# Optimization experiments

Measured on AMD Instinct MI355X. Metric: run time of the kernel, lower is better.

Reference implementation:

```python
import jax, jax.numpy as jnp
import numpy as np

B, N, D_POINTS, D_MODEL = 2, 2048, 32, 512


def _gather(feat, idx):
    # feat: [B, N, C], idx: [B, N, K] -> [B, N, K, C]
    return jax.vmap(lambda f, i: f[i])(feat, idx)


def setup_inputs() -> dict:
    key = jax.random.key(0)
    ks = jax.random.split(key, 20)
    def lin(k, fan_in, fan_out):
        bound = 1.0 / np.sqrt(fan_in)
        return jax.random.uniform(k, (fan_in, fan_out), jnp.float32, -bound, bound)
    def bias(k, fan_in, fan_out):
        bound = 1.0 / np.sqrt(fan_in)
        return jax.random.uniform(k, (fan_out,), jnp.float32, -bound, bound)
    return {
        "xyz": jax.random.normal(ks[0], (B, N, 3), jnp.float32),
        "points": jax.random.normal(ks[1], (B, N, D_POINTS), jnp.float32),
        "fc1_w": lin(ks[2], D_POINTS, D_MODEL), "fc1_b": bias(ks[3], D_POINTS, D_MODEL),
        "fc2_w": lin(ks[4], D_MODEL, D_POINTS), "fc2_b": bias(ks[5], D_MODEL, D_POINTS),
        "delta_w1": lin(ks[6], 3, D_MODEL), "delta_b1": bias(ks[7], 3, D_MODEL),
        "delta_w2": lin(ks[8], D_MODEL, D_MODEL), "delta_b2": bias(ks[9], D_MODEL, D_MODEL),
        "gamma_w1": lin(ks[10], D_MODEL, D_MODEL), "gamma_b1": bias(ks[11], D_MODEL, D_MODEL),
        "gamma_w2": lin(ks[12], D_MODEL, D_MODEL), "gamma_b2": bias(ks[13], D_MODEL, D_MODEL),
        "wq": lin(ks[14], D_MODEL, D_MODEL),
        "wk": lin(ks[15], D_MODEL, D_MODEL),
        "wv": lin(ks[16], D_MODEL, D_MODEL),
        "knn_k": 16,
    }


def reference(xyz, points, fc1_w, fc1_b, fc2_w, fc2_b,
              delta_w1, delta_b1, delta_w2, delta_b2,
              gamma_w1, gamma_b1, gamma_w2, gamma_b2,
              wq, wk, wv, knn_k):
    # square_distance: [B, N, N]
    sq = jnp.sum(xyz * xyz, axis=-1)
    dists = sq[:, :, None] + sq[:, None, :] - 2.0 * jnp.einsum('bnc,bmc->bnm', xyz, xyz)
    # knn: k smallest distances (argsort[:, :, :k] equivalent)
    _, knn_idx = jax.lax.top_k(-dists, knn_k)           # [B, N, K]
    knn_xyz = _gather(xyz, knn_idx)                      # [B, N, K, 3]

    pre = points
    x = points @ fc1_w + fc1_b                           # [B, N, d_model]
    q = x @ wq                                           # [B, N, d_model]
    k = _gather(x @ wk, knn_idx)                         # [B, N, K, d_model]
    v = _gather(x @ wv, knn_idx)                         # [B, N, K, d_model]

    # positional encoding MLP on delta xyz
    delta = xyz[:, :, None, :] - knn_xyz                 # [B, N, K, 3]
    pos_enc = jax.nn.relu(delta @ delta_w1 + delta_b1) @ delta_w2 + delta_b2

    # gamma MLP on (q - k + pos_enc)
    a = q[:, :, None, :] - k + pos_enc
    a = jax.nn.relu(a @ gamma_w1 + gamma_b1) @ gamma_w2 + gamma_b2

    scale = jnp.asarray(np.sqrt(D_MODEL), a.dtype)
    attn = jax.nn.softmax(a / scale, axis=-2)            # softmax over neighbors, per channel

    res = jnp.sum(attn * (v + pos_enc), axis=2)          # einsum 'bmnf,bmnf->bmf'
    res = res @ fc2_w + fc2_b + pre                      # [B, N, d_points]
    return res, attn
```

## Files before the change

kernel.cpp:

```cpp
#include <hip/hip_runtime.h>
#include <hip/hip_bf16.h>
#include <math.h>

typedef __bf16 bf16_t;
typedef float f32x4 __attribute__((ext_vector_type(4)));
typedef bf16_t bf16x8 __attribute__((ext_vector_type(8)));

#define BM 128
#define BN 128
#define BKT 32
#define NT 16

#define GLD_LDS16(gp, lp) __builtin_amdgcn_global_load_lds( \
    (const __attribute__((address_space(1))) void*)(gp), \
    (__attribute__((address_space(3))) void*)(lp), 16, 0, 0)

struct TC7 { const float* src[7]; bf16_t* dst[7]; };
__global__ __launch_bounds__(256) void tcast7_kernel(TC7 tc) {
  int job = blockIdx.x >> 10;
  int idx = (blockIdx.x & 1023) * 256 + threadIdx.x;
  if (job < 6) {
    int n = idx >> 9, k = idx & 511;
    tc.dst[job][idx] = (bf16_t)tc.src[job][k * 512 + n];
  } else {
    tc.dst[job][idx] = (bf16_t)tc.src[job][idx];
  }
}

__global__ __launch_bounds__(256) void cc_kernel(const float* __restrict__ db2, const float* __restrict__ gw1,
                                                 const float* __restrict__ gb1, float* __restrict__ cc) {
  int n = blockIdx.x * 256 + threadIdx.x;
  float s = gb1[n];
  for (int d = 0; d < 512; ++d) s = fmaf(db2[d], gw1[d * 512 + n], s);
  cc[n] = s;
}

__global__ __launch_bounds__(256) void knn_kernel(const float* __restrict__ xyz, int* __restrict__ knn) {
  __shared__ float sx[2048], sy[2048], sz[2048], sq[2048];
  int tid = threadIdx.x;
  int lane = tid & 63, wave = tid >> 6;
  int gq = blockIdx.x * 4 + wave;
  int b  = gq >> 11;
  int base = b << 11;
  for (int p = tid; p < 2048; p += 256) {
    float x = xyz[(base + p) * 3 + 0];
    float y = xyz[(base + p) * 3 + 1];
    float z = xyz[(base + p) * 3 + 2];
    sx[p] = x; sy[p] = y; sz[p] = z;
    sq[p] = __fadd_rn(__fadd_rn(__fmul_rn(x, x), __fmul_rn(y, y)), __fmul_rn(z, z));
  }
  __syncthreads();
  int iq = gq & 2047;
  float qx = sx[iq], qy = sy[iq], qz = sz[iq], sqi = sq[iq];

  unsigned long long key[32];
  #pragma unroll
  for (int j = 0; j < 32; ++j) {
    int p = lane + j * 64;
    float d = __fmul_rn(sx[p], qx);
    d = fmaf(sy[p], qy, d);
    d = fmaf(sz[p], qz, d);
    float dist = __fsub_rn(__fadd_rn(sqi, sq[p]), __fmul_rn(2.0f, d));
    unsigned int bits = __float_as_uint(dist);
    unsigned int sk = bits ^ (unsigned int)(((int)bits >> 31) | 0x80000000);
    key[j] = ((unsigned long long)sk << 32) | (unsigned int)p;
  }

  int r = 0;
  #pragma unroll 1
  for (int s = 0; s < 16; ++s) {
    unsigned long long m = key[0];
    #pragma unroll
    for (int j = 1; j < 32; ++j) m = (key[j] < m) ? key[j] : m;
    #pragma unroll
    for (int off = 32; off > 0; off >>= 1) {
      unsigned long long o = (unsigned long long)__shfl_xor((long long)m, off);
      if (o < m) m = o;
    }
    if (lane == s) r = base + (int)(m & 0xFFFFFFFFu);
    #pragma unroll
    for (int j = 0; j < 32; ++j) key[j] = (key[j] == m) ? ~0ULL : key[j];
  }
  if (lane < 16) knn[gq * 16 + lane] = r;
}

__global__ __launch_bounds__(256) void xfeat_kernel(const float* __restrict__ points, const float* __restrict__ fc1_w,
                                                    const float* __restrict__ fc1_b, bf16_t* __restrict__ xb) {
  __shared__ float p[32];
  int m = blockIdx.x, tid = threadIdx.x;
  if (tid < 32) p[tid] = points[m * 32 + tid];
  __syncthreads();
  for (int c = tid; c < 512; c += 256) {
    float a = fc1_b[c];
    #pragma unroll
    for (int kk = 0; kk < 32; ++kk) a = fmaf(p[kk], fc1_w[kk * 512 + c], a);
    xb[m * 512 + c] = (bf16_t)a;
  }
}

__global__ __launch_bounds__(256) void final_kernel(const float* __restrict__ res_mid, const float* __restrict__ fc2_w,
                                                    const float* __restrict__ fc2_b, const float* __restrict__ points,
                                                    float* __restrict__ out) {
  int oid = blockIdx.x * 256 + threadIdx.x;
  int m = oid >> 5, c = oid & 31;
  float a = fc2_b[c];
  const float* rm = res_mid + m * 512;
  for (int kk = 0; kk < 512; ++kk) a = fmaf(rm[kk], fc2_w[kk * 32 + c], a);
  out[oid] = a + points[oid];
}

struct GP {
  const bf16_t* A; const bf16_t* Bt; const bf16_t* Bt2;
  bf16_t* Cb; float* Cf; const float* bias; int ldc;
  const float* xyz; const int* knn; const float* dw1; const float* db1;
  const float* cc; const bf16_t* qkg;
  const bf16_t* vb; float* pe_attn; float* res_mid;
};

template <int SRC, int EPI>
__global__ __launch_bounds__(256) void gemm_kernel(GP gp) {
  __shared__ bf16_t Alds[2 * BM * BKT];
  __shared__ bf16_t Blds[2 * BN * BKT];
  __shared__ bf16_t B2lds[(EPI == 5) ? (2 * BN * BKT) : 8];
  __shared__ float  wl[(SRC == 2) ? 4 * 512 : 8];
  int tid  = threadIdx.x;
  int lane = tid & 63, wave = tid >> 6;
  int wr = wave >> 1, wc = wave & 1;
  int lr = lane & 15, lg = lane >> 4;

  int gx = gridDim.x;
  int nwg = gx * gridDim.y;
  int orig = blockIdx.y * gx + blockIdx.x;
  int cpx = nwg >> 3;
  int swz = (orig & 7) * cpx + (orig >> 3);
  int bx = swz % gx;
  int by = swz / gx;
  int n0 = bx * BN, m0 = by * BM;

  f32x4 acc[4][4];
  f32x4 acc2[(EPI == 5) ? 4 : 1][4];
  #pragma unroll
  for (int i = 0; i < 4; ++i)
    #pragma unroll
    for (int j = 0; j < 4; ++j) {
      acc[i][j] = (f32x4){0.f, 0.f, 0.f, 0.f};
      if (EPI == 5) acc2[i][j] = (f32x4){0.f, 0.f, 0.f, 0.f};
    }

  int rS2 = tid >> 2;
  int sl  = tid & 3;
  int swb = (rS2 >> 1) & 3;
  int scS = ((sl ^ swb) << 3);

  float dx0, dy0, dz0, dx1, dy1, dz1;
  if (SRC == 2) {
    for (int c = tid; c < 512; c += 256) {
      wl[c]        = gp.dw1[c];
      wl[512 + c]  = gp.dw1[512 + c];
      wl[1024 + c] = gp.dw1[1024 + c];
      wl[1536 + c] = gp.db1[c];
    }
    int m_a = m0 + rS2, m_b = m0 + rS2 + 64;
    int ga = m_a >> 4, ja = gp.knn[m_a];
    int gb = m_b >> 4, jb = gp.knn[m_b];
    dx0 = gp.xyz[ga * 3 + 0] - gp.xyz[ja * 3 + 0];
    dy0 = gp.xyz[ga * 3 + 1] - gp.xyz[ja * 3 + 1];
    dz0 = gp.xyz[ga * 3 + 2] - gp.xyz[ja * 3 + 2];
    dx1 = gp.xyz[gb * 3 + 0] - gp.xyz[jb * 3 + 0];
    dy1 = gp.xyz[gb * 3 + 1] - gp.xyz[jb * 3 + 1];
    dz1 = gp.xyz[gb * 3 + 2] - gp.xyz[jb * 3 + 2];
    __syncthreads();
  }

  auto stageA = [&](int t, int buf) {
    int k0 = t * BKT;
    if (SRC == 0) {
      GLD_LDS16(gp.A + (size_t)(m0 + rS2) * 512 + k0 + scS,       Alds + buf * (BM * BKT) + tid * 8);
      GLD_LDS16(gp.A + (size_t)(m0 + 64 + rS2) * 512 + k0 + scS,  Alds + buf * (BM * BKT) + 2048 + tid * 8);
    } else {
      int cb = k0 + sl * 8;
      f32x4 w0a = *(const f32x4*)(&wl[cb]),        w0b = *(const f32x4*)(&wl[cb + 4]);
      f32x4 w1a = *(const f32x4*)(&wl[512 + cb]),  w1b = *(const f32x4*)(&wl[512 + cb + 4]);
      f32x4 w2a = *(const f32x4*)(&wl[1024 + cb]), w2b = *(const f32x4*)(&wl[1024 + cb + 4]);
      f32x4 bba = *(const f32x4*)(&wl[1536 + cb]), bbb = *(const f32x4*)(&wl[1536 + cb + 4]);
      bf16_t* Ab = Alds + buf * (BM * BKT);
      bf16x8 o;
      #pragma unroll
      for (int u = 0; u < 4; ++u) {
        float h = fmaf(dz0, w2a[u], fmaf(dy0, w1a[u], dx0 * w0a[u])) + bba[u];
        o[u] = (bf16_t)fmaxf(h, 0.0f);
      }
      #pragma unroll
      for (int u = 0; u < 4; ++u) {
        float h = fmaf(dz0, w2b[u], fmaf(dy0, w1b[u], dx0 * w0b[u])) + bbb[u];
        o[4 + u] = (bf16_t)fmaxf(h, 0.0f);
      }
      *(bf16x8*)(&Ab[rS2 * BKT + ((sl ^ swb) << 3)]) = o;
      #pragma unroll
      for (int u = 0; u < 4; ++u) {
        float h = fmaf(dz1, w2a[u], fmaf(dy1, w1a[u], dx1 * w0a[u])) + bba[u];
        o[u] = (bf16_t)fmaxf(h, 0.0f);
      }
      #pragma unroll
      for (int u = 0; u < 4; ++u) {
        float h = fmaf(dz1, w2b[u], fmaf(dy1, w1b[u], dx1 * w0b[u])) + bbb[u];
        o[4 + u] = (bf16_t)fmaxf(h, 0.0f);
      }
      *(bf16x8*)(&Ab[(rS2 + 64) * BKT + ((sl ^ swb) << 3)]) = o;
    }
  };
  auto stageB = [&](int t, int buf) {
    int k0 = t * BKT;
    GLD_LDS16(gp.Bt + (size_t)(n0 + rS2) * 512 + k0 + scS,       Blds + buf * (BN * BKT) + tid * 8);
    GLD_LDS16(gp.Bt + (size_t)(n0 + 64 + rS2) * 512 + k0 + scS,  Blds + buf * (BN * BKT) + 2048 + tid * 8);
    if (EPI == 5) {
      GLD_LDS16(gp.Bt2 + (size_t)(n0 + rS2) * 512 + k0 + scS,      B2lds + buf * (BN * BKT) + tid * 8);
      GLD_LDS16(gp.Bt2 + (size_t)(n0 + 64 + rS2) * 512 + k0 + scS, B2lds + buf * (BN * BKT) + 2048 + tid * 8);
    }
  };

  stageA(0, 0);
  stageB(0, 0);

  #pragma unroll 1
  for (int t = 0; t < NT; ++t) {
    int cur = t & 1;
    if (t + 1 < NT) {
      stageA(t + 1, cur ^ 1);
      stageB(t + 1, cur ^ 1);
      if (SRC == 0) {
        if (EPI == 5) asm volatile("s_waitcnt vmcnt(6)" ::: "memory");
        else          asm volatile("s_waitcnt vmcnt(4)" ::: "memory");
      } else {
        if (EPI == 5) asm volatile("s_waitcnt vmcnt(4) lgkmcnt(0)" ::: "memory");
        else          asm volatile("s_waitcnt vmcnt(2) lgkmcnt(0)" ::: "memory");
      }
    } else {
      asm volatile("s_waitcnt vmcnt(0) lgkmcnt(0)" ::: "memory");
    }
    __builtin_amdgcn_s_barrier();

    const bf16_t* Ab = Alds + cur * (BM * BKT);
    const bf16_t* Bb = Blds + cur * (BN * BKT);
    const bf16_t* B2b = B2lds + cur * (BN * BKT);
    bf16x8 af[4], bfr[4], b2r[4];
    #pragma unroll
    for (int mi = 0; mi < 4; ++mi) {
      int rr = wr * 64 + mi * 16 + lr;
      af[mi] = *(const bf16x8*)(&Ab[rr * BKT + ((lg ^ ((rr >> 1) & 3)) << 3)]);
    }
    #pragma unroll
    for (int nj = 0; nj < 4; ++nj) {
      int rr = wc * 64 + nj * 16 + lr;
      bfr[nj] = *(const bf16x8*)(&Bb[rr * BKT + ((lg ^ ((rr >> 1) & 3)) << 3)]);
      if (EPI == 5) b2r[nj] = *(const bf16x8*)(&B2b[rr * BKT + ((lg ^ ((rr >> 1) & 3)) << 3)]);
    }
    #pragma unroll
    for (int mi = 0; mi < 4; ++mi)
      #pragma unroll
      for (int nj = 0; nj < 4; ++nj) {
        acc[mi][nj] = __builtin_amdgcn_mfma_f32_16x16x32_bf16(af[mi], bfr[nj], acc[mi][nj], 0, 0, 0);
        if (EPI == 5)
          acc2[mi][nj] = __builtin_amdgcn_mfma_f32_16x16x32_bf16(af[mi], b2r[nj], acc2[mi][nj], 0, 0, 0);
      }
    __builtin_amdgcn_s_barrier();
  }

  if (EPI == 4) {
    #pragma unroll
    for (int mi = 0; mi < 4; ++mi)
      #pragma unroll
      for (int nj = 0; nj < 4; ++nj) {
        int col = n0 + wc * 64 + nj * 16 + lr;
        #pragma unroll
        for (int r = 0; r < 4; ++r) {
          int row = m0 + wr * 64 + mi * 16 + lg * 4 + r;
          gp.Cb[(size_t)col * 512 + row] = (bf16_t)acc[mi][nj][r];
        }
      }
  } else if (EPI == 6) {
    #pragma unroll
    for (int mi = 0; mi < 4; ++mi)
      #pragma unroll
      for (int nj = 0; nj < 4; ++nj) {
        int col = n0 + wc * 64 + nj * 16 + lr;
        int part = col >> 9, c = col & 511;
        #pragma unroll
        for (int r = 0; r < 4; ++r) {
          int row = m0 + wr * 64 + mi * 16 + lg * 4 + r;
          gp.Cb[((size_t)part * 4096 + row) * 512 + c] = (bf16_t)acc[mi][nj][r];
        }
      }
  } else if (EPI == 7) {
    #pragma unroll
    for (int mi = 0; mi < 4; ++mi)
      #pragma unroll
      for (int nj = 0; nj < 4; ++nj) {
        int col = n0 + wc * 64 + nj * 16 + lr;
        #pragma unroll
        for (int r = 0; r < 4; ++r) {
          int row = m0 + wr * 64 + mi * 16 + lg * 4 + r;
          gp.Cb[(size_t)row * gp.ldc + col] = (bf16_t)acc[mi][nj][r];
        }
      }
  } else if (EPI == 5) {
    #pragma unroll
    for (int mi = 0; mi < 4; ++mi) {
      int g = (m0 + wr * 64 + mi * 16) >> 4;
      #pragma unroll
      for (int nj = 0; nj < 4; ++nj) {
        int col = n0 + wc * 64 + nj * 16 + lr;
        float db2v = gp.bias[col];
        float ccv  = gp.cc[col];
        float qgv  = (float)gp.qkg[(size_t)g * 512 + col];
        #pragma unroll
        for (int r = 0; r < 4; ++r) {
          int row = m0 + wr * 64 + mi * 16 + lg * 4 + r;
          gp.Cf[(size_t)row * 512 + col] = acc[mi][nj][r] + db2v;
          int j = gp.knn[row];
          float kgv = (float)gp.qkg[(size_t)(4096 + j) * 512 + col];
          float hv = acc2[mi][nj][r] + ccv + qgv - kgv;
          gp.Cb[(size_t)row * 512 + col] = (bf16_t)fmaxf(hv, 0.0f);
        }
      }
    }
  } else {
    const float scale = 22.62741699796952f;
    #pragma unroll
    for (int mi = 0; mi < 4; ++mi) {
      int g = (m0 + wr * 64 + mi * 16) >> 4;
      #pragma unroll
      for (int nj = 0; nj < 4; ++nj) {
        int col = n0 + wc * 64 + nj * 16 + lr;
        float sv[4];
        float mx = -INFINITY;
        #pragma unroll
        for (int r = 0; r < 4; ++r) {
          sv[r] = (acc[mi][nj][r] + gp.bias[col]) / scale;
          mx = fmaxf(mx, sv[r]);
        }
        mx = fmaxf(mx, __shfl_xor(mx, 16));
        mx = fmaxf(mx, __shfl_xor(mx, 32));
        float e[4], sum = 0.f;
        #pragma unroll
        for (int r = 0; r < 4; ++r) { e[r] = expf(sv[r] - mx); sum += e[r]; }
        sum += __shfl_xor(sum, 16);
        sum += __shfl_xor(sum, 32);
        float part = 0.f;
        #pragma unroll
        for (int r = 0; r < 4; ++r) {
          int row = g * 16 + lg * 4 + r;
          float at = e[r] / sum;
          int j = gp.knn[row];
          float vv  = (float)gp.vb[(size_t)j * 512 + col];
          float pev = gp.pe_attn[(size_t)row * 512 + col];
          part = fmaf(at, vv + pev, part);
          gp.pe_attn[(size_t)row * 512 + col] = at;
        }
        part += __shfl_xor(part, 16);
        part += __shfl_xor(part, 32);
        if (lg == 0) gp.res_mid[(size_t)g * 512 + col] = part;
      }
    }
  }
}

extern "C" void kernel_launch(void* const* d_in, const int* in_sizes, int n_in,
                              void* d_out, int out_size, void* d_ws, size_t ws_size,
                              hipStream_t stream) {
  const float* xyz    = (const float*)d_in[0];
  const float* points = (const float*)d_in[1];
  const float* fc1_w  = (const float*)d_in[2];
  const float* fc1_b  = (const float*)d_in[3];
  const float* fc2_w  = (const float*)d_in[4];
  const float* fc2_b  = (const float*)d_in[5];
  const float* dw1    = (const float*)d_in[6];
  const float* db1    = (const float*)d_in[7];
  const float* dw2    = (const float*)d_in[8];
  const float* db2    = (const float*)d_in[9];
  const float* gw1    = (const float*)d_in[10];
  const float* gb1    = (const float*)d_in[11];
  const float* gw2    = (const float*)d_in[12];
  const float* gb2    = (const float*)d_in[13];
  const float* wq     = (const float*)d_in[14];
  const float* wk     = (const float*)d_in[15];
  const float* wv     = (const float*)d_in[16];

  float* out = (float*)d_out;
  float* attn_pe = out + 131072;

  char* w = (char*)d_ws;
  bf16_t* wqkvT  = (bf16_t*)w; w += (size_t)1536 * 512 * 2;
  bf16_t* dw2T   = (bf16_t*)w; w += (size_t)512 * 512 * 2;
  bf16_t* gw1T   = (bf16_t*)w; w += (size_t)512 * 512 * 2;
  bf16_t* gw2T   = (bf16_t*)w; w += (size_t)512 * 512 * 2;
  bf16_t* dw2b   = (bf16_t*)w; w += (size_t)512 * 512 * 2;
  bf16_t* WpT    = (bf16_t*)w; w += (size_t)512 * 512 * 2;
  float*  cc     = (float*)w;  w += (size_t)512 * 4;
  int*    knn    = (int*)w;    w += (size_t)65536 * 4;
  bf16_t* xb     = (bf16_t*)w; w += (size_t)4096 * 512 * 2;
  bf16_t* qkvb   = (bf16_t*)w; w += (size_t)3 * 4096 * 512 * 2;
  bf16_t* qkg    = (bf16_t*)w; w += (size_t)2 * 4096 * 512 * 2;
  bf16_t* h2     = (bf16_t*)w; w += (size_t)65536 * 512 * 2;
  float*  res_mid= (float*)w;  w += (size_t)4096 * 512 * 4;

  TC7 tc;
  tc.src[0] = wq;  tc.dst[0] = wqkvT;
  tc.src[1] = wk;  tc.dst[1] = wqkvT + 512 * 512;
  tc.src[2] = wv;  tc.dst[2] = wqkvT + 2 * 512 * 512;
  tc.src[3] = dw2; tc.dst[3] = dw2T;
  tc.src[4] = gw1; tc.dst[4] = gw1T;
  tc.src[5] = gw2; tc.dst[5] = gw2T;
  tc.src[6] = dw2; tc.dst[6] = dw2b;
  tcast7_kernel<<<7168, 256, 0, stream>>>(tc);

  knn_kernel<<<1024, 256, 0, stream>>>(xyz, knn);
  xfeat_kernel<<<4096, 256, 0, stream>>>(points, fc1_w, fc1_b, xb);
  cc_kernel<<<2, 256, 0, stream>>>(db2, gw1, gb1, cc);

  GP gp{};
  gp.A = dw2b; gp.Bt = gw1T; gp.Cb = WpT; gp.ldc = 512;
  gemm_kernel<0, 4><<<dim3(4, 4), 256, 0, stream>>>(gp);

  GP gq{};
  gq.A = xb; gq.Bt = wqkvT; gq.Cb = qkvb; gq.ldc = 1536;
  gemm_kernel<0, 6><<<dim3(12, 32), 256, 0, stream>>>(gq);

  GP gk{};
  gk.A = qkvb; gk.Bt = gw1T; gk.Cb = qkg; gk.ldc = 512;
  gemm_kernel<0, 7><<<dim3(4, 64), 256, 0, stream>>>(gk);

  GP gd{};
  gd.Bt = dw2T; gd.Bt2 = WpT; gd.Cf = attn_pe; gd.Cb = h2; gd.bias = db2;
  gd.xyz = xyz; gd.knn = knn; gd.dw1 = dw1; gd.db1 = db1;
  gd.cc = cc; gd.qkg = qkg;
  gemm_kernel<2, 5><<<dim3(4, 512), 256, 0, stream>>>(gd);

  GP gs{};
  gs.A = h2; gs.Bt = gw2T; gs.bias = gb2;
  gs.knn = knn; gs.vb = qkvb + (size_t)2 * 4096 * 512; gs.pe_attn = attn_pe; gs.res_mid = res_mid;
  gemm_kernel<0, 3><<<dim3(4, 512), 256, 0, stream>>>(gs);

  final_kernel<<<512, 256, 0, stream>>>(res_mid, fc2_w, fc2_b, points, out);
}
```

Baseline: 504.9 us.

## Fold gamma_w1 into Wq/Wk weights and drop the separate qk-gamma GEMM

Precomputes Wq·Gw1 and Wk·Gw1 as weight products in the small batched weight GEMM (alongside dw2·Gw1), so the QKV GEMM directly emits v, q·Gw1 and k·Gw1. This removes the intermediate GEMM over the 4096-row q/k activations and its launch. The main loop is restructured: the SRC==2 path issues its computed A staging after the MFMA phase, with raised wave priority during the MFMAs, to overlap VALU with matrix work. Rounding the fused weight products to bf16 slightly changes numerics.

```diff
diff --git a/kernel.cpp b/kernel.cpp
--- a/kernel.cpp
+++ b/kernel.cpp
@@ -19,7 +19,7 @@
 __global__ __launch_bounds__(256) void tcast7_kernel(TC7 tc) {
   int job = blockIdx.x >> 10;
   int idx = (blockIdx.x & 1023) * 256 + threadIdx.x;
-  if (job < 6) {
+  if (job < 4) {
     int n = idx >> 9, k = idx & 511;
     tc.dst[job][idx] = (bf16_t)tc.src[job][k * 512 + n];
   } else {
@@ -115,6 +115,7 @@
   const float* xyz; const int* knn; const float* dw1; const float* db1;
   const float* cc; const bf16_t* qkg;
   const bf16_t* vb; float* pe_attn; float* res_mid;
+  const bf16_t* Aj[3]; bf16_t* Cbj[3];
 };
 
 template <int SRC, int EPI>
@@ -135,7 +136,9 @@
   int swz = (orig & 7) * cpx + (orig >> 3);
   int bx = swz % gx;
   int by = swz / gx;
-  int n0 = bx * BN, m0 = by * BM;
+  int n0 = bx * BN;
+  int m0 = ((EPI == 4) ? (by & 3) : by) * BM;
+  const bf16_t* Aptr = (EPI == 4) ? gp.Aj[by >> 2] : gp.A;
 
   f32x4 acc[4][4];
   f32x4 acc2[(EPI == 5) ? 4 : 1][4];
@@ -175,8 +178,8 @@
   auto stageA = [&](int t, int buf) {
     int k0 = t * BKT;
     if (SRC == 0) {
-      GLD_LDS16(gp.A + (size_t)(m0 + rS2) * 512 + k0 + scS,       Alds + buf * (BM * BKT) + tid * 8);
-      GLD_LDS16(gp.A + (size_t)(m0 + 64 + rS2) * 512 + k0 + scS,  Alds + buf * (BM * BKT) + 2048 + tid * 8);
+      GLD_LDS16(Aptr + (size_t)(m0 + rS2) * 512 + k0 + scS,       Alds + buf * (BM * BKT) + tid * 8);
+      GLD_LDS16(Aptr + (size_t)(m0 + 64 + rS2) * 512 + k0 + scS,  Alds + buf * (BM * BKT) + 2048 + tid * 8);
     } else {
       int cb = k0 + sl * 8;
       f32x4 w0a = *(const f32x4*)(&wl[cb]),        w0b = *(const f32x4*)(&wl[cb + 4]);
@@ -218,28 +221,7 @@
       GLD_LDS16(gp.Bt2 + (size_t)(n0 + 64 + rS2) * 512 + k0 + scS, B2lds + buf * (BN * BKT) + 2048 + tid * 8);
     }
   };
-
-  stageA(0, 0);
-  stageB(0, 0);
-
-  #pragma unroll 1
-  for (int t = 0; t < NT; ++t) {
-    int cur = t & 1;
-    if (t + 1 < NT) {
-      stageA(t + 1, cur ^ 1);
-      stageB(t + 1, cur ^ 1);
-      if (SRC == 0) {
-        if (EPI == 5) asm volatile("s_waitcnt vmcnt(6)" ::: "memory");
-        else          asm volatile("s_waitcnt vmcnt(4)" ::: "memory");
-      } else {
-        if (EPI == 5) asm volatile("s_waitcnt vmcnt(4) lgkmcnt(0)" ::: "memory");
-        else          asm volatile("s_waitcnt vmcnt(2) lgkmcnt(0)" ::: "memory");
-      }
-    } else {
-      asm volatile("s_waitcnt vmcnt(0) lgkmcnt(0)" ::: "memory");
-    }
-    __builtin_amdgcn_s_barrier();
-
+  auto mfmaPhase = [&](int cur) {
     const bf16_t* Ab = Alds + cur * (BM * BKT);
     const bf16_t* Bb = Blds + cur * (BN * BKT);
     const bf16_t* B2b = B2lds + cur * (BN * BKT);
@@ -263,10 +245,43 @@
         if (EPI == 5)
           acc2[mi][nj] = __builtin_amdgcn_mfma_f32_16x16x32_bf16(af[mi], b2r[nj], acc2[mi][nj], 0, 0, 0);
       }
-    __builtin_amdgcn_s_barrier();
+  };
+
+  stageA(0, 0);
+  stageB(0, 0);
+
+  #pragma unroll 1
+  for (int t = 0; t < NT; ++t) {
+    int cur = t & 1;
+    if (SRC == 0) {
+      if (t + 1 < NT) {
+        stageA(t + 1, cur ^ 1);
+        stageB(t + 1, cur ^ 1);
+        asm volatile("s_waitcnt vmcnt(4)" ::: "memory");
+      } else {
+        asm volatile("s_waitcnt vmcnt(0)" ::: "memory");
+      }
+      __builtin_amdgcn_s_barrier();
+      mfmaPhase(cur);
+      __builtin_amdgcn_s_barrier();
+    } else {
+      if (t + 1 < NT) {
+        stageB(t + 1, cur ^ 1);
+        asm volatile("s_waitcnt vmcnt(4) lgkmcnt(0)" ::: "memory");
+      } else {
+        asm volatile("s_waitcnt vmcnt(0) lgkmcnt(0)" ::: "memory");
+      }
+      __builtin_amdgcn_s_barrier();
+      __builtin_amdgcn_s_setprio(1);
+      mfmaPhase(cur);
+      __builtin_amdgcn_s_setprio(0);
+      if (t + 1 < NT) stageA(t + 1, cur ^ 1);
+      __builtin_amdgcn_s_barrier();
+    }
   }
 
   if (EPI == 4) {
+    bf16_t* CbT = gp.Cbj[by >> 2];
     #pragma unroll
     for (int mi = 0; mi < 4; ++mi)
       #pragma unroll
@@ -275,7 +290,7 @@
         #pragma unroll
         for (int r = 0; r < 4; ++r) {
           int row = m0 + wr * 64 + mi * 16 + lg * 4 + r;
-          gp.Cb[(size_t)col * 512 + row] = (bf16_t)acc[mi][nj][r];
+          CbT[(size_t)col * 512 + row] = (bf16_t)acc[mi][nj][r];
         }
       }
   } else if (EPI == 6) {
@@ -291,18 +306,6 @@
           gp.Cb[((size_t)part * 4096 + row) * 512 + c] = (bf16_t)acc[mi][nj][r];
         }
       }
-  } else if (EPI == 7) {
-    #pragma unroll
-    for (int mi = 0; mi < 4; ++mi)
-      #pragma unroll
-      for (int nj = 0; nj < 4; ++nj) {
-        int col = n0 + wc * 64 + nj * 16 + lr;
-        #pragma unroll
-        for (int r = 0; r < 4; ++r) {
-          int row = m0 + wr * 64 + mi * 16 + lg * 4 + r;
-          gp.Cb[(size_t)row * gp.ldc + col] = (bf16_t)acc[mi][nj][r];
-        }
-      }
   } else if (EPI == 5) {
     #pragma unroll
     for (int mi = 0; mi < 4; ++mi) {
@@ -312,13 +315,13 @@
         int col = n0 + wc * 64 + nj * 16 + lr;
         float db2v = gp.bias[col];
         float ccv  = gp.cc[col];
-        float qgv  = (float)gp.qkg[(size_t)g * 512 + col];
+        float qgv  = (float)gp.qkg[((size_t)4096 + g) * 512 + col];
         #pragma unroll
         for (int r = 0; r < 4; ++r) {
           int row = m0 + wr * 64 + mi * 16 + lg * 4 + r;
           gp.Cf[(size_t)row * 512 + col] = acc[mi][nj][r] + db2v;
           int j = gp.knn[row];
-          float kgv = (float)gp.qkg[(size_t)(4096 + j) * 512 + col];
+          float kgv = (float)gp.qkg[((size_t)2 * 4096 + j) * 512 + col];
           float hv = acc2[mi][nj][r] + ccv + qgv - kgv;
           gp.Cb[(size_t)row * 512 + col] = (bf16_t)fmaxf(hv, 0.0f);
         }
@@ -390,55 +393,55 @@
   float* attn_pe = out + 131072;
 
   char* w = (char*)d_ws;
-  bf16_t* wqkvT  = (bf16_t*)w; w += (size_t)1536 * 512 * 2;
+  bf16_t* wBig   = (bf16_t*)w; w += (size_t)1536 * 512 * 2;
   bf16_t* dw2T   = (bf16_t*)w; w += (size_t)512 * 512 * 2;
   bf16_t* gw1T   = (bf16_t*)w; w += (size_t)512 * 512 * 2;
   bf16_t* gw2T   = (bf16_t*)w; w += (size_t)512 * 512 * 2;
   bf16_t* dw2b   = (bf16_t*)w; w += (size_t)512 * 512 * 2;
+  bf16_t* wqb    = (bf16_t*)w; w += (size_t)512 * 512 * 2;
+  bf16_t* wkb    = (bf16_t*)w; w += (size_t)512 * 512 * 2;
   bf16_t* WpT    = (bf16_t*)w; w += (size_t)512 * 512 * 2;
   float*  cc     = (float*)w;  w += (size_t)512 * 4;
   int*    knn    = (int*)w;    w += (size_t)65536 * 4;
   bf16_t* xb     = (bf16_t*)w; w += (size_t)4096 * 512 * 2;
-  bf16_t* qkvb   = (bf16_t*)w; w += (size_t)3 * 4096 * 512 * 2;
-  bf16_t* qkg    = (bf16_t*)w; w += (size_t)2 * 4096 * 512 * 2;
+  bf16_t* vqkg   = (bf16_t*)w; w += (size_t)3 * 4096 * 512 * 2;
   bf16_t* h2     = (bf16_t*)w; w += (size_t)65536 * 512 * 2;
   float*  res_mid= (float*)w;  w += (size_t)4096 * 512 * 4;
 
   TC7 tc;
-  tc.src[0] = wq;  tc.dst[0] = wqkvT;
-  tc.src[1] = wk;  tc.dst[1] = wqkvT + 512 * 512;
-  tc.src[2] = wv;  tc.dst[2] = wqkvT + 2 * 512 * 512;
-  tc.src[3] = dw2; tc.dst[3] = dw2T;
-  tc.src[4] = gw1; tc.dst[4] = gw1T;
-  tc.src[5] = gw2; tc.dst[5] = gw2T;
-  tc.src[6] = dw2; tc.dst[6] = dw2b;
+  tc.src[0] = wv;  tc.dst[0] = wBig;
+  tc.src[1] = dw2; tc.dst[1] = dw2T;
+  tc.src[2] = gw1; tc.dst[2] = gw1T;
+  tc.src[3] = gw2; tc.dst[3] = gw2T;
+  tc.src[4] = dw2; tc.dst[4] = dw2b;
+  tc.src[5] = wq;  tc.dst[5] = wqb;
+  tc.src[6] = wk;  tc.dst[6] = wkb;
   tcast7_kernel<<<7168, 256, 0, stream>>>(tc);
 
   knn_kernel<<<1024, 256, 0, stream>>>(xyz, knn);
   xfeat_kernel<<<4096, 256, 0, stream>>>(points, fc1_w, fc1_b, xb);
   cc_kernel<<<2, 256, 0, stream>>>(db2, gw1, gb1, cc);
 
-  GP gp{};
-  gp.A = dw2b; gp.Bt = gw1T; gp.Cb = WpT; gp.ldc = 512;
-  gemm_kernel<0, 4><<<dim3(4, 4), 256, 0, stream>>>(gp);
+  GP gwp{};
+  gwp.Bt = gw1T;
+  gwp.Aj[0] = dw2b; gwp.Cbj[0] = WpT;
+  gwp.Aj[1] = wqb;  gwp.Cbj[1] = wBig + (size_t)512 * 512;
+  gwp.Aj[2] = wkb;  gwp.Cbj[2] = wBig + (size_t)2 * 512 * 512;
+  gemm_kernel<0, 4><<<dim3(4, 12), 256, 0, stream>>>(gwp);
 
   GP gq{};
-  gq.A = xb; gq.Bt = wqkvT; gq.Cb = qkvb; gq.ldc = 1536;
+  gq.A = xb; gq.Bt = wBig; gq.Cb = vqkg; gq.ldc = 1536;
   gemm_kernel<0, 6><<<dim3(12, 32), 256, 0, stream>>>(gq);
-
-  GP gk{};
-  gk.A = qkvb; gk.Bt = gw1T; gk.Cb = qkg; gk.ldc = 512;
-  gemm_kernel<0, 7><<<dim3(4, 64), 256, 0, stream>>>(gk);
 
   GP gd{};
   gd.Bt = dw2T; gd.Bt2 = WpT; gd.Cf = attn_pe; gd.Cb = h2; gd.bias = db2;
   gd.xyz = xyz; gd.knn = knn; gd.dw1 = dw1; gd.db1 = db1;
-  gd.cc = cc; gd.qkg = qkg;
+  gd.cc = cc; gd.qkg = vqkg;
   gemm_kernel<2, 5><<<dim3(4, 512), 256, 0, stream>>>(gd);
 
   GP gs{};
   gs.A = h2; gs.Bt = gw2T; gs.bias = gb2;
-  gs.knn = knn; gs.vb = qkvb + (size_t)2 * 4096 * 512; gs.pe_attn = attn_pe; gs.res_mid = res_mid;
+  gs.knn = knn; gs.vb = vqkg; gs.pe_attn = attn_pe; gs.res_mid = res_mid;
   gemm_kernel<0, 3><<<dim3(4, 512), 256, 0, stream>>>(gs);
 
   final_kernel<<<512, 256, 0, stream>>>(res_mid, fc2_w, fc2_b, points, out);
```

Measured after the change: 501.2 us. About the same (-0.7%).
